# Performance work log

Hardware: AMD Instinct MI355X
Metric: run time of the kernel (lower is better)

## Reference

```python
import jax, jax.numpy as jnp
import numpy as np

B, N, F_IN, F_OUT = 16, 1024, 128, 128
LEAKY_SLOPE = 0.01  # torch nn.LeakyReLU default


def setup_inputs() -> dict:
    key = jax.random.key(0)
    k1, k2, k3, k4 = jax.random.split(key, 4)
    node_mat = jax.random.normal(k1, (B, N, F_IN), dtype=jnp.float32)
    adj_mat = jax.random.uniform(k2, (B, N, N), dtype=jnp.float32)
    # nn.Linear(node_in_len, node_out_len): weight [F_OUT, F_IN], bias [F_OUT]
    bound = 1.0 / np.sqrt(F_IN)
    W = jax.random.uniform(k3, (F_OUT, F_IN), minval=-bound, maxval=bound, dtype=jnp.float32)
    b = jax.random.uniform(k4, (F_OUT,), minval=-bound, maxval=bound, dtype=jnp.float32)
    return {"node_mat": node_mat, "adj_mat": adj_mat, "W": W, "b": b}


def reference(node_mat, adj_mat, W, b):
    # degree normalization: row-scale adjacency by 1/degree
    # (the torch code builds a diagonal inv-degree matrix and bmm's it;
    #  mathematically identical to a broadcast row scale)
    n_neighbors = adj_mat.sum(axis=-1, keepdims=True)          # [B, N, 1]
    norm_adj = adj_mat / n_neighbors                           # [B, N, N]
    node_fea = jnp.einsum('bnm,bmf->bnf', norm_adj, node_mat)  # [B, N, F_in]
    node_fea = jnp.einsum('bnf,of->bno', node_fea, W) + b      # linear
    return jnp.where(node_fea >= 0, node_fea, LEAKY_SLOPE * node_fea)
```

## Files before the change

### kernel.cpp

```cpp
#include <hip/hip_runtime.h>
#include <hip/hip_bf16.h>


typedef __attribute__((ext_vector_type(8))) __bf16 bf16x8;
typedef __attribute__((ext_vector_type(4))) float f32x4;

#define GLD16(gp, lp) __builtin_amdgcn_global_load_lds( \
    (const __attribute__((address_space(1))) unsigned int*)(gp), \
    (__attribute__((address_space(3))) unsigned int*)(lp), 16, 0, 0)

__device__ __forceinline__ unsigned f2bf_pk(float lo, float hi) {
    union { float f; unsigned u; } a, b;
    a.f = lo; b.f = hi;
    unsigned ra = (a.u + 0x7FFFu + ((a.u >> 16) & 1u)) >> 16;
    unsigned rb = (b.u + 0x7FFFu + ((b.u >> 16) & 1u)) & 0xFFFF0000u;
    return ra | rb;
}

__device__ __forceinline__ bf16x8 cvt8(const f32x4& a, const f32x4& b) {
    union { unsigned u[4]; bf16x8 v; } r;
    r.u[0] = f2bf_pk(a.x, a.y);
    r.u[1] = f2bf_pk(a.z, a.w);
    r.u[2] = f2bf_pk(b.x, b.y);
    r.u[3] = f2bf_pk(b.z, b.w);
    return r.v;
}

__global__ __launch_bounds__(256, 2)
void k1_xw(const float* __restrict__ x, const float* __restrict__ W,
           unsigned short* __restrict__ yF)
{
    __shared__ unsigned short Ax[64 * 128];
    __shared__ unsigned short Bw[128 * 128];

    const int t   = threadIdx.x;
    const int bid = blockIdx.x;
    const int xcd = bid & 7;
    const int j   = bid >> 3;
    const int b   = xcd * 2 + (j >> 4);
    const int m0  = (j & 15) << 6;
    const float* xb = x + (((long)b << 10) + m0) * 128;

#pragma unroll
    for (int i = 0; i < 8; ++i) {
        int e = i * 1024 + t * 4;
        int r = e >> 7, f = e & 127;
        f32x4 v = *(const f32x4*)(xb + (long)r * 128 + f);
        int c = f >> 3;
        int byte = r * 256 + (((c ^ (r & 7)) << 4) | ((f & 7) << 1));
        uint2 pk; pk.x = f2bf_pk(v.x, v.y); pk.y = f2bf_pk(v.z, v.w);
        *(uint2*)((char*)Ax + byte) = pk;
    }
#pragma unroll
    for (int i = 0; i < 16; ++i) {
        int e = i * 1024 + t * 4;
        int r = e >> 7, f = e & 127;
        f32x4 v = *(const f32x4*)(W + r * 128 + f);
        int c = f >> 3;
        int byte = r * 256 + (((c ^ (r & 7)) << 4) | ((f & 7) << 1));
        uint2 pk; pk.x = f2bf_pk(v.x, v.y); pk.y = f2bf_pk(v.z, v.w);
        *(uint2*)((char*)Bw + byte) = pk;
    }
    __syncthreads();

    const int lane = t & 63, w = t >> 6;
    const int lrow = lane & 15, lq = lane >> 4;

    bf16x8 af[4];
#pragma unroll
    for (int kk = 0; kk < 4; ++kk) {
        int r = w * 16 + lrow;
        int c = kk * 4 + lq;
        af[kk] = *(const bf16x8*)((const char*)Ax + r * 256 + ((c ^ (r & 7)) << 4));
    }

    f32x4 zero = {0.f, 0.f, 0.f, 0.f};
    f32x4 acc[8] = {zero, zero, zero, zero, zero, zero, zero, zero};
#pragma unroll
    for (int nf = 0; nf < 8; ++nf) {
#pragma unroll
        for (int kk = 0; kk < 4; ++kk) {
            int o = nf * 16 + lrow;
            int c = kk * 4 + lq;
            bf16x8 bfrag = *(const bf16x8*)((const char*)Bw + o * 256 + ((c ^ (o & 7)) << 4));
            acc[nf] = __builtin_amdgcn_mfma_f32_16x16x32_bf16(af[kk], bfrag, acc[nf], 0, 0, 0);
        }
    }

    {
        const int ks = (m0 >> 5) + (w >> 1);
        const int q  = (w & 1) * 2 + (lq >> 1);
        const int jb = (lq & 1) * 4;
#pragma unroll
        for (int nf = 0; nf < 8; ++nf) {
            uint2 pk;
            pk.x = f2bf_pk(acc[nf][0], acc[nf][1]);
            pk.y = f2bf_pk(acc[nf][2], acc[nf][3]);
            long off = (((long)((b * 32 + ks) * 8 + nf)) << 9) + (q * 16 + lrow) * 8 + jb;
            *(uint2*)(yF + off) = pk;
        }
    }
}

__global__ __launch_bounds__(512, 2)
void k2_agg(const float* __restrict__ adj, const unsigned short* __restrict__ yF,
            const float* __restrict__ bias, float* __restrict__ out)
{
    __shared__ float          bufA[2][64 * 128];
    __shared__ unsigned short bufY[2][32 * 512];

    const int bid = blockIdx.x;
    const int xcd = bid & 7;
    const int j   = bid >> 3;
    const int b   = xcd * 2 + (j >> 4);
    const int n0  = (j & 15) << 6;

    const int t = threadIdx.x;
    const int lane = t & 63, w = t >> 6;
    const int h = w >> 1, oc = w & 1;
    const int lrow = lane & 15, lq = lane >> 4;

    const float* adjb = adj + ((long)b << 20);

    const int srow = (lane >> 5);
    const int ssc  = lane & 31;

    f32x4 zero = {0.f, 0.f, 0.f, 0.f};
    f32x4 acc[4] = {zero, zero, zero, zero};
    float dsum = 0.f;

#define STAGE(BUF, S)                                                                  \
    do {                                                                               \
        if (w < 4) {                                                                   \
            _Pragma("unroll")                                                          \
            for (int i = 0; i < 8; ++i) {                                              \
                int rl = w * 16 + 2 * i + srow;                                        \
                const float* g = adjb + ((long)(n0 + rl) << 10) + (S) * 128            \
                               + ((ssc ^ (rl & 7)) << 2);                              \
                GLD16(g, &bufA[BUF][(w * 16 + 2 * i) * 128]);                          \
            }                                                                          \
        } else {                                                                       \
            const int ks = w - 4;                                                      \
            _Pragma("unroll")                                                          \
            for (int i = 0; i < 8; ++i) {                                              \
                const unsigned short* g = yF                                           \
                    + (((long)((b * 32 + (S) * 4 + ks) * 8 + i)) << 9) + lane * 8;     \
                GLD16(g, &bufY[BUF][(ks * 8 + i) << 9]);                               \
            }                                                                          \
        }                                                                              \
    } while (0)

    STAGE(0, 0);
    __syncthreads();

    for (int s = 0; s < 8; ++s) {
        const int cur = s & 1;
        if (s < 7) STAGE(cur ^ 1, s + 1);

        const int row = h * 16 + lrow;
        const int rx  = row & 7;
#pragma unroll
        for (int kk = 0; kk < 4; ++kk) {
            const int c0 = kk * 8 + lq * 2;
            f32x4 a0 = *(const f32x4*)&bufA[cur][row * 128 + ((c0 ^ rx) << 2)];
            f32x4 a1 = *(const f32x4*)&bufA[cur][row * 128 + (((c0 + 1) ^ rx) << 2)];
            dsum += a0.x + a0.y + a0.z + a0.w + a1.x + a1.y + a1.z + a1.w;
            bf16x8 a = cvt8(a0, a1);
#pragma unroll
            for (int n = 0; n < 4; ++n) {
                const int ot = oc * 4 + n;
                bf16x8 bb = *(const bf16x8*)&bufY[cur][((kk * 8 + ot) << 9) + lane * 8];
                acc[n] = __builtin_amdgcn_mfma_f32_16x16x32_bf16(a, bb, acc[n], 0, 0, 0);
            }
        }
        __syncthreads();
    }

    dsum += __shfl_xor(dsum, 16, 64);
    dsum += __shfl_xor(dsum, 32, 64);
    float invd[4];
#pragma unroll
    for (int i = 0; i < 4; ++i)
        invd[i] = 1.0f / __shfl(dsum, lq * 4 + i, 64);

#pragma unroll
    for (int n = 0; n < 4; ++n) {
        const int o = (oc * 4 + n) * 16 + lrow;
        const float bv = bias[o];
#pragma unroll
        for (int i = 0; i < 4; ++i) {
            const int r = n0 + h * 16 + lq * 4 + i;
            float v = acc[n][i] * invd[i] + bv;
            v = (v >= 0.f) ? v : 0.01f * v;
            out[(((long)(b * 1024 + r)) << 7) + o] = v;
        }
    }
#undef STAGE
}

extern "C" void kernel_launch(void* const* d_in, const int* in_sizes, int n_in,
                              void* d_out, int out_size, void* d_ws, size_t ws_size,
                              hipStream_t stream) {
    const float* node = (const float*)d_in[0];
    const float* adj  = (const float*)d_in[1];
    const float* W    = (const float*)d_in[2];
    const float* bias = (const float*)d_in[3];
    float* out = (float*)d_out;
    unsigned short* yF = (unsigned short*)d_ws;

    k1_xw<<<dim3(256), dim3(256), 0, stream>>>(node, W, yF);
    k2_agg<<<dim3(256), dim3(512), 0, stream>>>(adj, yF, bias, out);
}
```

Measured before the change: 28.83 us.

## Split XW kernel into smaller tiles and balance k2 loads with explicit vmcnt waits

Result: slower. 36.15 us (+25.4%).

```diff
diff --git a/kernel.cpp b/kernel.cpp
--- a/kernel.cpp
+++ b/kernel.cpp
@@ -8,6 +8,12 @@
 #define GLD16(gp, lp) __builtin_amdgcn_global_load_lds( \
     (const __attribute__((address_space(1))) unsigned int*)(gp), \
     (__attribute__((address_space(3))) unsigned int*)(lp), 16, 0, 0)
+
+#define WAITV8()  do { asm volatile("s_waitcnt vmcnt(8)" ::: "memory"); \
+                       __builtin_amdgcn_sched_barrier(0); } while (0)
+#define WAITV0()  do { asm volatile("s_waitcnt vmcnt(0)" ::: "memory"); \
+                       __builtin_amdgcn_sched_barrier(0); } while (0)
+#define BAR()     __builtin_amdgcn_s_barrier()
 
 __device__ __forceinline__ unsigned f2bf_pk(float lo, float hi) {
     union { float f; unsigned u; } a, b;
@@ -26,23 +32,21 @@
     return r.v;
 }
 
-__global__ __launch_bounds__(256, 2)
+__global__ __launch_bounds__(256, 4)
 void k1_xw(const float* __restrict__ x, const float* __restrict__ W,
            unsigned short* __restrict__ yF)
 {
-    __shared__ unsigned short Ax[64 * 128];
+    __shared__ unsigned short Ax[16 * 128];
     __shared__ unsigned short Bw[128 * 128];
 
-    const int t   = threadIdx.x;
-    const int bid = blockIdx.x;
-    const int xcd = bid & 7;
-    const int j   = bid >> 3;
-    const int b   = xcd * 2 + (j >> 4);
-    const int m0  = (j & 15) << 6;
+    const int t  = threadIdx.x;
+    const int wg = blockIdx.x;
+    const int b  = wg >> 6;
+    const int m0 = (wg & 63) << 4;
     const float* xb = x + (((long)b << 10) + m0) * 128;
 
 #pragma unroll
-    for (int i = 0; i < 8; ++i) {
+    for (int i = 0; i < 2; ++i) {
         int e = i * 1024 + t * 4;
         int r = e >> 7, f = e & 127;
         f32x4 v = *(const f32x4*)(xb + (long)r * 128 + f);
@@ -69,18 +73,18 @@
     bf16x8 af[4];
 #pragma unroll
     for (int kk = 0; kk < 4; ++kk) {
-        int r = w * 16 + lrow;
+        int r = lrow;
         int c = kk * 4 + lq;
         af[kk] = *(const bf16x8*)((const char*)Ax + r * 256 + ((c ^ (r & 7)) << 4));
     }
 
     f32x4 zero = {0.f, 0.f, 0.f, 0.f};
-    f32x4 acc[8] = {zero, zero, zero, zero, zero, zero, zero, zero};
-#pragma unroll
-    for (int nf = 0; nf < 8; ++nf) {
+    f32x4 acc[2] = {zero, zero};
+#pragma unroll
+    for (int nf = 0; nf < 2; ++nf) {
 #pragma unroll
         for (int kk = 0; kk < 4; ++kk) {
-            int o = nf * 16 + lrow;
+            int o = (w * 2 + nf) * 16 + lrow;
             int c = kk * 4 + lq;
             bf16x8 bfrag = *(const bf16x8*)((const char*)Bw + o * 256 + ((c ^ (o & 7)) << 4));
             acc[nf] = __builtin_amdgcn_mfma_f32_16x16x32_bf16(af[kk], bfrag, acc[nf], 0, 0, 0);
@@ -88,15 +92,16 @@
     }
 
     {
-        const int ks = (m0 >> 5) + (w >> 1);
-        const int q  = (w & 1) * 2 + (lq >> 1);
+        const int ks = m0 >> 5;
+        const int q  = ((m0 >> 4) & 1) * 2 + (lq >> 1);
         const int jb = (lq & 1) * 4;
 #pragma unroll
-        for (int nf = 0; nf < 8; ++nf) {
+        for (int nf = 0; nf < 2; ++nf) {
+            int ot = w * 2 + nf;
             uint2 pk;
             pk.x = f2bf_pk(acc[nf][0], acc[nf][1]);
             pk.y = f2bf_pk(acc[nf][2], acc[nf][3]);
-            long off = (((long)((b * 32 + ks) * 8 + nf)) << 9) + (q * 16 + lrow) * 8 + jb;
+            long off = (((long)((b * 32 + ks) * 8 + ot)) << 9) + (q * 16 + lrow) * 8 + jb;
             *(uint2*)(yF + off) = pk;
         }
     }
@@ -131,49 +136,56 @@
 
 #define STAGE(BUF, S)                                                                  \
     do {                                                                               \
-        if (w < 4) {                                                                   \
+        _Pragma("unroll")                                                              \
+        for (int i = 0; i < 4; ++i) {                                                  \
+            int rl = w * 8 + 2 * i + srow;                                             \
+            const float* g = adjb + ((long)(n0 + rl) << 10) + (S) * 128                \
+                           + ((ssc ^ (rl & 7)) << 2);                                  \
+            GLD16(g, &bufA[BUF][(w * 8 + 2 * i) * 128]);                               \
+        }                                                                              \
+        _Pragma("unroll")                                                              \
+        for (int i2 = 0; i2 < 4; ++i2) {                                               \
+            int f = w * 4 + i2;                                                        \
+            const unsigned short* g = yF                                               \
+                + (((long)((b * 32 + (S) * 4 + (f >> 3)) * 8 + (f & 7))) << 9)         \
+                + lane * 8;                                                            \
+            GLD16(g, &bufY[BUF][f << 9]);                                              \
+        }                                                                              \
+    } while (0)
+
+#define COMPUTE(BUF)                                                                   \
+    do {                                                                               \
+        const int row = h * 16 + lrow;                                                 \
+        const int rx  = row & 7;                                                       \
+        _Pragma("unroll")                                                              \
+        for (int kk = 0; kk < 4; ++kk) {                                               \
+            const int c0 = kk * 8 + lq * 2;                                            \
+            f32x4 a0 = *(const f32x4*)&bufA[BUF][row * 128 + ((c0 ^ rx) << 2)];        \
+            f32x4 a1 = *(const f32x4*)&bufA[BUF][row * 128 + (((c0 + 1) ^ rx) << 2)];  \
+            dsum += a0.x + a0.y + a0.z + a0.w + a1.x + a1.y + a1.z + a1.w;             \
+            bf16x8 a = cvt8(a0, a1);                                                   \
             _Pragma("unroll")                                                          \
-            for (int i = 0; i < 8; ++i) {                                              \
-                int rl = w * 16 + 2 * i + srow;                                        \
-                const float* g = adjb + ((long)(n0 + rl) << 10) + (S) * 128            \
-                               + ((ssc ^ (rl & 7)) << 2);                              \
-                GLD16(g, &bufA[BUF][(w * 16 + 2 * i) * 128]);                          \
-            }                                                                          \
-        } else {                                                                       \
-            const int ks = w - 4;                                                      \
-            _Pragma("unroll")                                                          \
-            for (int i = 0; i < 8; ++i) {                                              \
-                const unsigned short* g = yF                                           \
-                    + (((long)((b * 32 + (S) * 4 + ks) * 8 + i)) << 9) + lane * 8;     \
-                GLD16(g, &bufY[BUF][(ks * 8 + i) << 9]);                               \
+            for (int n = 0; n < 4; ++n) {                                              \
+                const int ot = oc * 4 + n;                                             \
+                bf16x8 bb = *(const bf16x8*)&bufY[BUF][((kk * 8 + ot) << 9) + lane * 8];\
+                acc[n] = __builtin_amdgcn_mfma_f32_16x16x32_bf16(a, bb, acc[n], 0, 0, 0);\
             }                                                                          \
         }                                                                              \
     } while (0)
 
     STAGE(0, 0);
-    __syncthreads();
-
+#pragma unroll
     for (int s = 0; s < 8; ++s) {
         const int cur = s & 1;
-        if (s < 7) STAGE(cur ^ 1, s + 1);
-
-        const int row = h * 16 + lrow;
-        const int rx  = row & 7;
-#pragma unroll
-        for (int kk = 0; kk < 4; ++kk) {
-            const int c0 = kk * 8 + lq * 2;
-            f32x4 a0 = *(const f32x4*)&bufA[cur][row * 128 + ((c0 ^ rx) << 2)];
-            f32x4 a1 = *(const f32x4*)&bufA[cur][row * 128 + (((c0 + 1) ^ rx) << 2)];
-            dsum += a0.x + a0.y + a0.z + a0.w + a1.x + a1.y + a1.z + a1.w;
-            bf16x8 a = cvt8(a0, a1);
-#pragma unroll
-            for (int n = 0; n < 4; ++n) {
-                const int ot = oc * 4 + n;
-                bf16x8 bb = *(const bf16x8*)&bufY[cur][((kk * 8 + ot) << 9) + lane * 8];
-                acc[n] = __builtin_amdgcn_mfma_f32_16x16x32_bf16(a, bb, acc[n], 0, 0, 0);
-            }
-        }
-        __syncthreads();
+        if (s < 7) {
+            STAGE(cur ^ 1, s + 1);
+            WAITV8();
+        } else {
+            WAITV0();
+        }
+        BAR();
+        COMPUTE(cur);
+        BAR();
     }
 
     dsum += __shfl_xor(dsum, 16, 64);
@@ -196,6 +208,7 @@
         }
     }
 #undef STAGE
+#undef COMPUTE
 }
 
 extern "C" void kernel_launch(void* const* d_in, const int* in_sizes, int n_in,
@@ -208,6 +221,6 @@
     float* out = (float*)d_out;
     unsigned short* yF = (unsigned short*)d_ws;
 
-    k1_xw<<<dim3(256), dim3(256), 0, stream>>>(node, W, yF);
+    k1_xw<<<dim3(1024), dim3(256), 0, stream>>>(node, W, yF);
     k2_agg<<<dim3(256), dim3(512), 0, stream>>>(adj, yF, bias, out);
 }
```
